# Kernel tuning notes

Hardware: AMD Instinct MI355X
Metric: run time of the kernel (lower is better)

The kernel has to match this reference:

```python
import jax, jax.numpy as jnp
import numpy as np

N = 50000     # nodes
E = 600000    # directed edges (avg degree 12)
F_IN = 128    # num_features
H = 128       # hidden_units
C = 16        # num_classes
G = 500       # graphs in batch


def setup_inputs() -> dict:
    key = jax.random.key(0)
    ks = jax.random.split(key, 6)
    x = jax.random.normal(ks[0], (N, F_IN), jnp.float32)
    edge_src = jax.random.randint(ks[1], (E,), 0, N, jnp.int32)
    edge_dst = jax.random.randint(ks[2], (E,), 0, N, jnp.int32)
    batch = jnp.sort(jax.random.randint(ks[3], (N,), 0, G, jnp.int32))
    W1 = jax.random.normal(ks[4], (F_IN, H), jnp.float32) / np.float32(np.sqrt(F_IN))
    b1 = jnp.zeros((H,), jnp.float32)
    W2 = jax.random.normal(ks[5], (H, C), jnp.float32) / np.float32(np.sqrt(H))
    b2 = jnp.zeros((C,), jnp.float32)
    return {"x": x, "W1": W1, "b1": b1, "W2": W2, "b2": b2,
            "edge_src": edge_src, "edge_dst": edge_dst, "batch": batch}


def _gcn_conv(x, W, b, src, dst, norm):
    # linear transform then normalized scatter-add aggregation (PyG GCNConv)
    h = x @ W                                   # [N, out]
    msg = h[src] * norm[:, None]                # [E+N, out]
    return jax.ops.segment_sum(msg, dst, num_segments=N) + b


def reference(x, W1, b1, W2, b2, edge_src, edge_dst, batch):
    # add self-loops
    loops = jnp.arange(N, dtype=edge_src.dtype)
    src = jnp.concatenate([edge_src, loops])
    dst = jnp.concatenate([edge_dst, loops])
    # symmetric normalization D^-1/2 A D^-1/2 (in-degree at targets)
    deg = jax.ops.segment_sum(jnp.ones_like(dst, jnp.float32), dst, num_segments=N)
    dis = jax.lax.rsqrt(deg)  # deg >= 1 because of self-loops
    norm = dis[src] * dis[dst]

    h = jax.nn.relu(_gcn_conv(x, W1, b1, src, dst, norm))
    h = _gcn_conv(h, W2, b2, src, dst, norm)

    # scatter_mean pooling over graphs
    counts = jax.ops.segment_sum(jnp.ones((N,), jnp.float32), batch, num_segments=G)
    pooled = jax.ops.segment_sum(h, batch, num_segments=G) / jnp.maximum(counts, 1.0)[:, None]
    return jax.nn.log_softmax(pooled, axis=1)
```

## Files before the change

### kernel.cpp

```cpp
#include <hip/hip_runtime.h>
#include <hip/hip_bf16.h>


#define NN 50000
#define EE 600000
#define FIN 128
#define HH 128
#define CC 16
#define GG 500
#define ETOT (EE + NN)
#define SBLK 196
#define WTS 140

typedef unsigned short ushort_t;
typedef unsigned int uint_t;

typedef __attribute__((ext_vector_type(8))) short bf16x8;
typedef __attribute__((ext_vector_type(8))) ushort_t u16x8;
typedef __attribute__((ext_vector_type(4))) ushort_t u16x4;
typedef __attribute__((ext_vector_type(4))) float f32x4;
typedef __attribute__((ext_vector_type(2))) float f32x2;

__device__ inline ushort_t f2bf(float f) {
    uint_t u = __float_as_uint(f);
    u = (u + 0x7FFFu + ((u >> 16) & 1u)) >> 16;
    return (ushort_t)u;
}
__device__ inline float bf2f(ushort_t b) {
    return __uint_as_float(((uint_t)b) << 16);
}
__device__ inline ushort_t f2h(float f) {
    _Float16 h = (_Float16)f; ushort_t u; __builtin_memcpy(&u, &h, 2); return u;
}
__device__ inline float h2f(ushort_t u) {
    _Float16 h; __builtin_memcpy(&h, &u, 2); return (float)h;
}

__global__ void init_kernel(int* cnt, float* pooled) {
    int i = blockIdx.x * blockDim.x + threadIdx.x;
    if (i < NN) cnt[i] = 0;
    if (i < GG * CC) pooled[i] = 0.0f;
}

__global__ void count_kernel(const int* __restrict__ edge_dst,
                             int* __restrict__ cnt, int* __restrict__ seq) {
    int idx = blockIdx.x * blockDim.x + threadIdx.x;
    if (idx < EE) seq[idx] = atomicAdd(&cnt[edge_dst[idx]], 1);
}

__global__ __launch_bounds__(256) void gemm1_kernel(const float* __restrict__ x,
                                                    const float* __restrict__ W1,
                                                    unsigned char* __restrict__ hb8) {
    __shared__ ushort_t xs[64 * 136];
    __shared__ ushort_t wt[128 * WTS];
    int t = threadIdx.x;
    int row0 = blockIdx.x * 64;
    for (int i = 0; i < 8; i++) {
        int slot = t + i * 256;
        int r = slot >> 5, k4 = slot & 31;
        int gr = row0 + r;
        float4 v = (gr < NN) ? ((const float4*)x)[gr * 32 + k4]
                             : make_float4(0.f, 0.f, 0.f, 0.f);
        u16x4 bv = { f2bf(v.x), f2bf(v.y), f2bf(v.z), f2bf(v.w) };
        *(u16x4*)(&xs[r * 136 + k4 * 4]) = bv;
    }
    for (int i = 0; i < 16; i++) {
        int idx = t + i * 256;
        int c = idx & 127, k4 = idx >> 7;
        u16x4 bv = { f2bf(W1[(4 * k4 + 0) * HH + c]),
                     f2bf(W1[(4 * k4 + 1) * HH + c]),
                     f2bf(W1[(4 * k4 + 2) * HH + c]),
                     f2bf(W1[(4 * k4 + 3) * HH + c]) };
        *(u16x4*)(&wt[c * WTS + k4 * 4]) = bv;
    }
    __syncthreads();

    int wave = t >> 6, lane = t & 63;
    int m = lane & 15, quad = lane >> 4;
    f32x4 acc[8];
    for (int ct = 0; ct < 8; ct++) acc[ct] = (f32x4)(0.0f);
    for (int ko = 0; ko < 4; ko++) {
        bf16x8 a = *(const bf16x8*)(&xs[(16 * wave + m) * 136 + ko * 32 + quad * 8]);
        for (int ct = 0; ct < 8; ct++) {
            bf16x8 b = *(const bf16x8*)(&wt[(ct * 16 + m) * WTS + ko * 32 + quad * 8]);
            acc[ct] = __builtin_amdgcn_mfma_f32_16x16x32_bf16(a, b, acc[ct], 0, 0, 0);
        }
    }
    for (int ct = 0; ct < 8; ct++) {
        int gcol = ct * 16 + m;
        for (int r = 0; r < 4; r++) {
            int grow = row0 + wave * 16 + quad * 4 + r;
            if (grow < NN) {
                int p = __builtin_amdgcn_cvt_pk_fp8_f32(acc[ct][r], 0.0f, 0, false);
                hb8[(size_t)grow * HH + gcol] = (unsigned char)(p & 0xFF);
            }
        }
    }
}

__device__ inline int block_excl_scan(int v, int t, int* total) {
    __shared__ int wsum[4];
    int lane = t & 63, wv = t >> 6;
    int inc = v;
    for (int off = 1; off < 64; off <<= 1) {
        int n = __shfl_up(inc, off);
        if (lane >= off) inc += n;
    }
    if (lane == 63) wsum[wv] = inc;
    __syncthreads();
    int off_w = 0;
    for (int w = 0; w < wv; w++) off_w += wsum[w];
    *total = wsum[0] + wsum[1] + wsum[2] + wsum[3];
    return off_w + inc - v;
}

__global__ __launch_bounds__(256) void scanA_kernel(const int* __restrict__ cnt,
                                                    int* __restrict__ rowptr,
                                                    float* __restrict__ dis,
                                                    int* __restrict__ bsum) {
    int t = threadIdx.x;
    int i = blockIdx.x * 256 + t;
    int d = 0;
    if (i < NN) {
        d = cnt[i] + 1;
        dis[i] = rsqrtf((float)d);
    }
    int total;
    int excl = block_excl_scan(d, t, &total);
    if (i < NN) rowptr[i] = excl;
    if (t == 0) bsum[blockIdx.x] = total;
}

__global__ __launch_bounds__(256) void scanBC_kernel(int* __restrict__ rowptr,
                                                     const int* __restrict__ bsum) {
    __shared__ int sb[256];
    int t = threadIdx.x;
    int v = (t < SBLK) ? bsum[t] : 0;
    int total;
    int ex = block_excl_scan(v, t, &total);
    sb[t] = ex;
    __syncthreads();
    int myoff = sb[blockIdx.x];
    int i = blockIdx.x * 256 + t;
    if (i < NN) rowptr[i] += myoff;
    if (blockIdx.x == 0 && t == 0) rowptr[NN] = ETOT;
}

__global__ void fill_kernel(const int* __restrict__ edge_src,
                            const int* __restrict__ edge_dst,
                            const float* __restrict__ dis,
                            const int* __restrict__ rowptr,
                            const int* __restrict__ seq,
                            uint_t* __restrict__ csr) {
    int idx = blockIdx.x * blockDim.x + threadIdx.x;
    if (idx < EE) {
        int s = edge_src[idx], d = edge_dst[idx];
        csr[rowptr[d] + seq[idx]] = (uint_t)s | ((uint_t)f2h(dis[s]) << 16);
    } else if (idx < ETOT) {
        int n = idx - EE;
        csr[rowptr[n + 1] - 1] = (uint_t)n | ((uint_t)f2h(dis[n]) << 16);
    }
}

__global__ __launch_bounds__(256) void agg1_kernel(const unsigned char* __restrict__ hb8,
                                                   const int* __restrict__ rowptr,
                                                   const uint_t* __restrict__ csr,
                                                   const float* __restrict__ dis,
                                                   const float* __restrict__ b1,
                                                   ushort_t* __restrict__ h1b) {
    int wave = threadIdx.x >> 6, lane = threadIdx.x & 63;
    int node = blockIdx.x * 4 + wave;
    int slot = lane >> 3, sub = lane & 7;
    int e0 = rowptr[node], e1 = rowptr[node + 1];
    float acc[16];
    for (int j = 0; j < 16; j++) acc[j] = 0.0f;
    for (int e = e0 + slot; e < e1; e += 16) {
        uint_t ent0 = csr[e];
        bool has2 = (e + 8) < e1;
        uint_t ent1 = has2 ? csr[e + 8] : ent0;
        uint4 hv0 = *(const uint4*)(hb8 + (size_t)(ent0 & 0xFFFFu) * HH + sub * 16);
        uint4 hv1 = has2 ? *(const uint4*)(hb8 + (size_t)(ent1 & 0xFFFFu) * HH + sub * 16)
                         : make_uint4(0, 0, 0, 0);
        float w0 = h2f((ushort_t)(ent0 >> 16));
        uint_t words0[4] = { hv0.x, hv0.y, hv0.z, hv0.w };
        for (int q = 0; q < 4; q++) {
            f32x2 lo = __builtin_amdgcn_cvt_pk_f32_fp8(words0[q], false);
            f32x2 hi = __builtin_amdgcn_cvt_pk_f32_fp8(words0[q], true);
            acc[q * 4 + 0] += w0 * lo[0];
            acc[q * 4 + 1] += w0 * lo[1];
            acc[q * 4 + 2] += w0 * hi[0];
            acc[q * 4 + 3] += w0 * hi[1];
        }
        if (has2) {
            float w1 = h2f((ushort_t)(ent1 >> 16));
            uint_t words1[4] = { hv1.x, hv1.y, hv1.z, hv1.w };
            for (int q = 0; q < 4; q++) {
                f32x2 lo = __builtin_amdgcn_cvt_pk_f32_fp8(words1[q], false);
                f32x2 hi = __builtin_amdgcn_cvt_pk_f32_fp8(words1[q], true);
                acc[q * 4 + 0] += w1 * lo[0];
                acc[q * 4 + 1] += w1 * lo[1];
                acc[q * 4 + 2] += w1 * hi[0];
                acc[q * 4 + 3] += w1 * hi[1];
            }
        }
    }
    for (int j = 0; j < 16; j++) {
        acc[j] += __shfl_xor(acc[j], 8);
        acc[j] += __shfl_xor(acc[j], 16);
        acc[j] += __shfl_xor(acc[j], 32);
    }
    if (slot == 0) {
        float dn = dis[node];
        const float4* b1v = (const float4*)(b1 + sub * 16);
        float4 bb[4] = { b1v[0], b1v[1], b1v[2], b1v[3] };
        const float* bbf = (const float*)bb;
        u16x8 o0, o1;
        for (int j = 0; j < 8; j++) {
            o0[j] = f2bf(fmaxf(dn * acc[j]     + bbf[j],     0.0f));
            o1[j] = f2bf(fmaxf(dn * acc[8 + j] + bbf[8 + j], 0.0f));
        }
        *(u16x8*)(h1b + (size_t)node * HH + sub * 16)     = o0;
        *(u16x8*)(h1b + (size_t)node * HH + sub * 16 + 8) = o1;
    }
}

__global__ __launch_bounds__(256) void gemm2_kernel(const ushort_t* __restrict__ h1b,
                                                    const float* __restrict__ W2,
                                                    ushort_t* __restrict__ h2b) {
    __shared__ ushort_t w2t[CC * 132];
    int t = threadIdx.x;
    for (int i = t; i < HH * CC; i += 256) {
        int k = i >> 4, m = i & 15;
        w2t[m * 132 + k] = f2bf(W2[i]);
    }
    __syncthreads();
    int wave = t >> 6, lane = t & 63;
    int m = lane & 15, quad = lane >> 4;
    int node0 = (blockIdx.x * 4 + wave) * 16;
    f32x4 acc = (f32x4)(0.0f);
    int arow = node0 + m;
    for (int ko = 0; ko < 4; ko++) {
        bf16x8 a = *(const bf16x8*)(h1b + (size_t)arow * HH + ko * 32 + quad * 8);
        bf16x8 b = *(const bf16x8*)(&w2t[m * 132 + ko * 32 + quad * 8]);
        acc = __builtin_amdgcn_mfma_f32_16x16x32_bf16(a, b, acc, 0, 0, 0);
    }
    for (int r = 0; r < 4; r++) {
        int grow = node0 + quad * 4 + r;
        h2b[(size_t)grow * CC + m] = f2bf(acc[r]);
    }
}

__global__ __launch_bounds__(1024) void agg2pool_kernel(const ushort_t* __restrict__ h2b,
                                                        const int* __restrict__ rowptr,
                                                        const uint_t* __restrict__ csr,
                                                        const float* __restrict__ dis,
                                                        const float* __restrict__ b2,
                                                        const int* __restrict__ batch,
                                                        float* __restrict__ pooled) {
    __shared__ float vals[16][16];
    __shared__ int gid[16];
    int wave = threadIdx.x >> 6, lane = threadIdx.x & 63;
    int node = blockIdx.x * 16 + wave;
    int slot = lane >> 3, sub = lane & 7;
    int e0 = rowptr[node], e1 = rowptr[node + 1];
    float a0 = 0.0f, a1 = 0.0f;
    for (int e = e0 + slot; e < e1; e += 16) {
        uint_t ent0 = csr[e];
        bool has2 = (e + 8) < e1;
        uint_t ent1 = has2 ? csr[e + 8] : ent0;
        uint_t p0 = *(const uint_t*)(h2b + (size_t)(ent0 & 0xFFFFu) * CC + sub * 2);
        uint_t p1 = has2 ? *(const uint_t*)(h2b + (size_t)(ent1 & 0xFFFFu) * CC + sub * 2) : 0;
        float w0 = h2f((ushort_t)(ent0 >> 16));
        a0 += w0 * bf2f((ushort_t)(p0 & 0xFFFFu));
        a1 += w0 * bf2f((ushort_t)(p0 >> 16));
        if (has2) {
            float w1 = h2f((ushort_t)(ent1 >> 16));
            a0 += w1 * bf2f((ushort_t)(p1 & 0xFFFFu));
            a1 += w1 * bf2f((ushort_t)(p1 >> 16));
        }
    }
    a0 += __shfl_xor(a0, 8); a0 += __shfl_xor(a0, 16); a0 += __shfl_xor(a0, 32);
    a1 += __shfl_xor(a1, 8); a1 += __shfl_xor(a1, 16); a1 += __shfl_xor(a1, 32);
    if (slot == 0) {
        float dn = dis[node];
        vals[wave][2 * sub]     = a0 * dn + b2[2 * sub];
        vals[wave][2 * sub + 1] = a1 * dn + b2[2 * sub + 1];
        if (sub == 0) gid[wave] = batch[node];
    }
    __syncthreads();
    if (threadIdx.x < 16) {
        int c = threadIdx.x;
        float run = 0.0f;
        for (int i = 0; i < 16; i++) {
            run += vals[i][c];
            if (i == 15 || gid[i + 1] != gid[i]) {
                atomicAdd(&pooled[gid[i] * CC + c], run);
                run = 0.0f;
            }
        }
    }
}

__global__ void lsm_kernel(const float* __restrict__ pooled,
                           const int* __restrict__ batch,
                           float* __restrict__ out) {
    int idx = blockIdx.x * blockDim.x + threadIdx.x;
    int g = idx >> 4, c = idx & 15;
    if (g >= GG) return;
    int lo = 0, hi = NN;
    while (lo < hi) { int mid = (lo + hi) >> 1; if (batch[mid] < g) lo = mid + 1; else hi = mid; }
    int lo2 = lo, hi2 = NN;
    while (lo2 < hi2) { int mid = (lo2 + hi2) >> 1; if (batch[mid] < g + 1) lo2 = mid + 1; else hi2 = mid; }
    float cnt = (float)(lo2 - lo);
    float v = pooled[g * CC + c] / fmaxf(cnt, 1.0f);
    float m = v;
    for (int off = 8; off >= 1; off >>= 1) m = fmaxf(m, __shfl_xor(m, off, 16));
    float s = expf(v - m);
    for (int off = 8; off >= 1; off >>= 1) s += __shfl_xor(s, off, 16);
    out[g * CC + c] = v - m - logf(s);
}

extern "C" void kernel_launch(void* const* d_in, const int* in_sizes, int n_in,
                              void* d_out, int out_size, void* d_ws, size_t ws_size,
                              hipStream_t stream) {
    const float* x  = (const float*)d_in[0];
    const float* W1 = (const float*)d_in[1];
    const float* b1 = (const float*)d_in[2];
    const float* W2 = (const float*)d_in[3];
    const float* b2 = (const float*)d_in[4];
    const int* edge_src = (const int*)d_in[5];
    const int* edge_dst = (const int*)d_in[6];
    const int* batch    = (const int*)d_in[7];
    float* out = (float*)d_out;

    char* ws = (char*)d_ws;
    size_t off = 0;
    auto alloc = [&](size_t bytes) {
        void* p = ws + off;
        off += (bytes + 255) & ~size_t(255);
        return p;
    };
    int*   cnt     = (int*)  alloc(NN * 4);
    float* dis     = (float*)alloc(NN * 4);
    int*   rowptr  = (int*)  alloc((NN + 1) * 4);
    int*   seq     = (int*)  alloc(EE * 4);
    int*   bsum    = (int*)  alloc(SBLK * 4);
    uint_t* csr    = (uint_t*)alloc((size_t)ETOT * 4);
    unsigned char* hb8 = (unsigned char*)alloc((size_t)NN * HH);
    ushort_t* h1b  = (ushort_t*)alloc((size_t)NN * HH * 2);
    ushort_t* h2b  = (ushort_t*)alloc((size_t)NN * CC * 2);
    float* pooled  = (float*)alloc(GG * CC * 4);

    const int B = 256;
    init_kernel<<<(NN + B - 1) / B, B, 0, stream>>>(cnt, pooled);
    count_kernel<<<(EE + B - 1) / B, B, 0, stream>>>(edge_dst, cnt, seq);
    gemm1_kernel<<<(NN + 63) / 64, B, 0, stream>>>(x, W1, hb8);
    scanA_kernel<<<SBLK, B, 0, stream>>>(cnt, rowptr, dis, bsum);
    scanBC_kernel<<<SBLK, B, 0, stream>>>(rowptr, bsum);
    fill_kernel<<<(ETOT + B - 1) / B, B, 0, stream>>>(edge_src, edge_dst, dis,
                                                      rowptr, seq, csr);
    agg1_kernel<<<NN / 4, B, 0, stream>>>(hb8, rowptr, csr, dis, b1, h1b);
    gemm2_kernel<<<(NN + 63) / 64, B, 0, stream>>>(h1b, W2, h2b);
    agg2pool_kernel<<<NN / 16, 1024, 0, stream>>>(h2b, rowptr, csr, dis, b2, batch, pooled);
    lsm_kernel<<<(GG * CC + B - 1) / B, B, 0, stream>>>(pooled, batch, out);
}
```

Before: 199.9 us.

## Fuse layer-1 aggregation with layer-2 GEMM and precompute graph counts

Merges agg1 and gemm2 into one kernel. Each 4-node block writes its bf16 hidden rows to shared memory and wave 0 runs the 16x16 MFMA against W2 staged in LDS. This removes the 12.8 MB h1b round trip through global memory and one kernel launch. In exchange, every block now converts W2 and runs an MFMA that is only a quarter full (4 of 16 rows), which adds per-block work and a barrier. Graph counts are now accumulated with atomics in count_kernel instead of binary searches in lsm_kernel, and a few loads in agg2pool are hoisted ahead of the edge loop.

```diff
diff --git a/kernel.cpp b/kernel.cpp
--- a/kernel.cpp
+++ b/kernel.cpp
@@ -36,16 +36,20 @@
     _Float16 h; __builtin_memcpy(&h, &u, 2); return (float)h;
 }
 
-__global__ void init_kernel(int* cnt, float* pooled) {
+__global__ void init_kernel(int* cnt, float* pooled, int* gcnt) {
     int i = blockIdx.x * blockDim.x + threadIdx.x;
     if (i < NN) cnt[i] = 0;
     if (i < GG * CC) pooled[i] = 0.0f;
+    if (i < GG) gcnt[i] = 0;
 }
 
 __global__ void count_kernel(const int* __restrict__ edge_dst,
-                             int* __restrict__ cnt, int* __restrict__ seq) {
+                             const int* __restrict__ batch,
+                             int* __restrict__ cnt, int* __restrict__ seq,
+                             int* __restrict__ gcnt) {
     int idx = blockIdx.x * blockDim.x + threadIdx.x;
     if (idx < EE) seq[idx] = atomicAdd(&cnt[edge_dst[idx]], 1);
+    if (idx < NN) atomicAdd(&gcnt[batch[idx]], 1);
 }
 
 __global__ __launch_bounds__(256) void gemm1_kernel(const float* __restrict__ x,
@@ -162,16 +166,21 @@
     }
 }
 
-__global__ __launch_bounds__(256) void agg1_kernel(const unsigned char* __restrict__ hb8,
-                                                   const int* __restrict__ rowptr,
-                                                   const uint_t* __restrict__ csr,
-                                                   const float* __restrict__ dis,
-                                                   const float* __restrict__ b1,
-                                                   ushort_t* __restrict__ h1b) {
-    int wave = threadIdx.x >> 6, lane = threadIdx.x & 63;
+__global__ __launch_bounds__(256) void agg1g2_kernel(const unsigned char* __restrict__ hb8,
+                                                     const int* __restrict__ rowptr,
+                                                     const uint_t* __restrict__ csr,
+                                                     const float* __restrict__ dis,
+                                                     const float* __restrict__ b1,
+                                                     const float* __restrict__ W2,
+                                                     ushort_t* __restrict__ h2b) {
+    __shared__ ushort_t h1s[16 * 136];
+    __shared__ ushort_t w2t[CC * 132];
+    int t = threadIdx.x;
+    int wave = t >> 6, lane = t & 63;
     int node = blockIdx.x * 4 + wave;
     int slot = lane >> 3, sub = lane & 7;
     int e0 = rowptr[node], e1 = rowptr[node + 1];
+    float dn = dis[node];
     float acc[16];
     for (int j = 0; j < 16; j++) acc[j] = 0.0f;
     for (int e = e0 + slot; e < e1; e += 16) {
@@ -204,13 +213,16 @@
             }
         }
     }
+    for (int i = t; i < HH * CC; i += 256) {
+        int k = i >> 4, m = i & 15;
+        w2t[m * 132 + k] = f2bf(W2[i]);
+    }
     for (int j = 0; j < 16; j++) {
         acc[j] += __shfl_xor(acc[j], 8);
         acc[j] += __shfl_xor(acc[j], 16);
         acc[j] += __shfl_xor(acc[j], 32);
     }
     if (slot == 0) {
-        float dn = dis[node];
         const float4* b1v = (const float4*)(b1 + sub * 16);
         float4 bb[4] = { b1v[0], b1v[1], b1v[2], b1v[3] };
         const float* bbf = (const float*)bb;
@@ -219,34 +231,24 @@
             o0[j] = f2bf(fmaxf(dn * acc[j]     + bbf[j],     0.0f));
             o1[j] = f2bf(fmaxf(dn * acc[8 + j] + bbf[8 + j], 0.0f));
         }
-        *(u16x8*)(h1b + (size_t)node * HH + sub * 16)     = o0;
-        *(u16x8*)(h1b + (size_t)node * HH + sub * 16 + 8) = o1;
-    }
-}
-
-__global__ __launch_bounds__(256) void gemm2_kernel(const ushort_t* __restrict__ h1b,
-                                                    const float* __restrict__ W2,
-                                                    ushort_t* __restrict__ h2b) {
-    __shared__ ushort_t w2t[CC * 132];
-    int t = threadIdx.x;
-    for (int i = t; i < HH * CC; i += 256) {
-        int k = i >> 4, m = i & 15;
-        w2t[m * 132 + k] = f2bf(W2[i]);
-    }
-    __syncthreads();
-    int wave = t >> 6, lane = t & 63;
-    int m = lane & 15, quad = lane >> 4;
-    int node0 = (blockIdx.x * 4 + wave) * 16;
-    f32x4 acc = (f32x4)(0.0f);
-    int arow = node0 + m;
-    for (int ko = 0; ko < 4; ko++) {
-        bf16x8 a = *(const bf16x8*)(h1b + (size_t)arow * HH + ko * 32 + quad * 8);
-        bf16x8 b = *(const bf16x8*)(&w2t[m * 132 + ko * 32 + quad * 8]);
-        acc = __builtin_amdgcn_mfma_f32_16x16x32_bf16(a, b, acc, 0, 0, 0);
-    }
-    for (int r = 0; r < 4; r++) {
-        int grow = node0 + quad * 4 + r;
-        h2b[(size_t)grow * CC + m] = f2bf(acc[r]);
+        *(u16x8*)(&h1s[wave * 136 + sub * 16])     = o0;
+        *(u16x8*)(&h1s[wave * 136 + sub * 16 + 8]) = o1;
+    }
+    __syncthreads();
+    if (wave == 0) {
+        int m = lane & 15, quad = lane >> 4;
+        f32x4 acc2 = (f32x4)(0.0f);
+        for (int ko = 0; ko < 4; ko++) {
+            bf16x8 a = *(const bf16x8*)(&h1s[m * 136 + ko * 32 + quad * 8]);
+            bf16x8 b = *(const bf16x8*)(&w2t[m * 132 + ko * 32 + quad * 8]);
+            acc2 = __builtin_amdgcn_mfma_f32_16x16x32_bf16(a, b, acc2, 0, 0, 0);
+        }
+        if (quad == 0) {
+            int node0 = blockIdx.x * 4;
+            for (int r = 0; r < 4; r++) {
+                h2b[(size_t)(node0 + r) * CC + m] = f2bf(acc2[r]);
+            }
+        }
     }
 }
 
@@ -263,6 +265,9 @@
     int node = blockIdx.x * 16 + wave;
     int slot = lane >> 3, sub = lane & 7;
     int e0 = rowptr[node], e1 = rowptr[node + 1];
+    float dn = dis[node];
+    int   bg = batch[node];
+    float b20 = b2[2 * sub], b21 = b2[2 * sub + 1];
     float a0 = 0.0f, a1 = 0.0f;
     for (int e = e0 + slot; e < e1; e += 16) {
         uint_t ent0 = csr[e];
@@ -282,10 +287,9 @@
     a0 += __shfl_xor(a0, 8); a0 += __shfl_xor(a0, 16); a0 += __shfl_xor(a0, 32);
     a1 += __shfl_xor(a1, 8); a1 += __shfl_xor(a1, 16); a1 += __shfl_xor(a1, 32);
     if (slot == 0) {
-        float dn = dis[node];
-        vals[wave][2 * sub]     = a0 * dn + b2[2 * sub];
-        vals[wave][2 * sub + 1] = a1 * dn + b2[2 * sub + 1];
-        if (sub == 0) gid[wave] = batch[node];
+        vals[wave][2 * sub]     = a0 * dn + b20;
+        vals[wave][2 * sub + 1] = a1 * dn + b21;
+        if (sub == 0) gid[wave] = bg;
     }
     __syncthreads();
     if (threadIdx.x < 16) {
@@ -302,16 +306,12 @@
 }
 
 __global__ void lsm_kernel(const float* __restrict__ pooled,
-                           const int* __restrict__ batch,
+                           const int* __restrict__ gcnt,
                            float* __restrict__ out) {
     int idx = blockIdx.x * blockDim.x + threadIdx.x;
     int g = idx >> 4, c = idx & 15;
     if (g >= GG) return;
-    int lo = 0, hi = NN;
-    while (lo < hi) { int mid = (lo + hi) >> 1; if (batch[mid] < g) lo = mid + 1; else hi = mid; }
-    int lo2 = lo, hi2 = NN;
-    while (lo2 < hi2) { int mid = (lo2 + hi2) >> 1; if (batch[mid] < g + 1) lo2 = mid + 1; else hi2 = mid; }
-    float cnt = (float)(lo2 - lo);
+    float cnt = (float)gcnt[g];
     float v = pooled[g * CC + c] / fmaxf(cnt, 1.0f);
     float m = v;
     for (int off = 8; off >= 1; off >>= 1) m = fmaxf(m, __shfl_xor(m, off, 16));
@@ -347,20 +347,19 @@
     int*   bsum    = (int*)  alloc(SBLK * 4);
     uint_t* csr    = (uint_t*)alloc((size_t)ETOT * 4);
     unsigned char* hb8 = (unsigned char*)alloc((size_t)NN * HH);
-    ushort_t* h1b  = (ushort_t*)alloc((size_t)NN * HH * 2);
     ushort_t* h2b  = (ushort_t*)alloc((size_t)NN * CC * 2);
     float* pooled  = (float*)alloc(GG * CC * 4);
+    int*   gcnt    = (int*)  alloc(GG * 4);
 
     const int B = 256;
-    init_kernel<<<(NN + B - 1) / B, B, 0, stream>>>(cnt, pooled);
-    count_kernel<<<(EE + B - 1) / B, B, 0, stream>>>(edge_dst, cnt, seq);
+    init_kernel<<<(NN + B - 1) / B, B, 0, stream>>>(cnt, pooled, gcnt);
+    count_kernel<<<(EE + B - 1) / B, B, 0, stream>>>(edge_dst, batch, cnt, seq, gcnt);
     gemm1_kernel<<<(NN + 63) / 64, B, 0, stream>>>(x, W1, hb8);
     scanA_kernel<<<SBLK, B, 0, stream>>>(cnt, rowptr, dis, bsum);
     scanBC_kernel<<<SBLK, B, 0, stream>>>(rowptr, bsum);
     fill_kernel<<<(ETOT + B - 1) / B, B, 0, stream>>>(edge_src, edge_dst, dis,
                                                       rowptr, seq, csr);
-    agg1_kernel<<<NN / 4, B, 0, stream>>>(hb8, rowptr, csr, dis, b1, h1b);
-    gemm2_kernel<<<(NN + 63) / 64, B, 0, stream>>>(h1b, W2, h2b);
+    agg1g2_kernel<<<NN / 4, B, 0, stream>>>(hb8, rowptr, csr, dis, b1, W2, h2b);
     agg2pool_kernel<<<NN / 16, 1024, 0, stream>>>(h2b, rowptr, csr, dis, b2, batch, pooled);
-    lsm_kernel<<<(GG * CC + B - 1) / B, B, 0, stream>>>(pooled, batch, out);
-}
+    lsm_kernel<<<(GG * CC + B - 1) / B, B, 0, stream>>>(pooled, gcnt, out);
+}
```

Result: slower. 224.1 us (+12.1%).

## Fuse edge counting into GEMM1 launch and precompute graph boundaries in scan

Applied to the files above, without the earlier changes.

Merges the degree-count atomics and the first GEMM into one heterogeneous launch, so the block ranges run concurrently and one kernel launch is removed. Graph start offsets are computed in the scan kernel, replacing two binary searches per thread in the log-softmax kernel. Loads of dis, batch and bias are hoisted before the aggregation loops, and gemm2 stores gain a bounds guard, with the buffers padded to match. The fused kernel now gives every block, including the counting blocks, the GEMM's large shared-memory allocation, which may reduce occupancy for the atomic part.

```diff
diff --git a/kernel.cpp b/kernel.cpp
--- a/kernel.cpp
+++ b/kernel.cpp
@@ -11,6 +11,7 @@
 #define ETOT (EE + NN)
 #define SBLK 196
 #define WTS 140
+#define CBLK ((EE + 255) / 256)
 
 typedef unsigned short ushort_t;
 typedef unsigned int uint_t;
@@ -42,19 +43,21 @@
     if (i < GG * CC) pooled[i] = 0.0f;
 }
 
-__global__ void count_kernel(const int* __restrict__ edge_dst,
-                             int* __restrict__ cnt, int* __restrict__ seq) {
-    int idx = blockIdx.x * blockDim.x + threadIdx.x;
-    if (idx < EE) seq[idx] = atomicAdd(&cnt[edge_dst[idx]], 1);
-}
-
-__global__ __launch_bounds__(256) void gemm1_kernel(const float* __restrict__ x,
-                                                    const float* __restrict__ W1,
-                                                    unsigned char* __restrict__ hb8) {
+__global__ __launch_bounds__(256) void cg1_kernel(const int* __restrict__ edge_dst,
+                                                  int* __restrict__ cnt,
+                                                  int* __restrict__ seq,
+                                                  const float* __restrict__ x,
+                                                  const float* __restrict__ W1,
+                                                  unsigned char* __restrict__ hb8) {
     __shared__ ushort_t xs[64 * 136];
     __shared__ ushort_t wt[128 * WTS];
+    if (blockIdx.x < CBLK) {
+        int idx = blockIdx.x * 256 + threadIdx.x;
+        if (idx < EE) seq[idx] = atomicAdd(&cnt[edge_dst[idx]], 1);
+        return;
+    }
     int t = threadIdx.x;
-    int row0 = blockIdx.x * 64;
+    int row0 = (blockIdx.x - CBLK) * 64;
     for (int i = 0; i < 8; i++) {
         int slot = t + i * 256;
         int r = slot >> 5, k4 = slot & 31;
@@ -117,13 +120,21 @@
 __global__ __launch_bounds__(256) void scanA_kernel(const int* __restrict__ cnt,
                                                     int* __restrict__ rowptr,
                                                     float* __restrict__ dis,
-                                                    int* __restrict__ bsum) {
+                                                    int* __restrict__ bsum,
+                                                    const int* __restrict__ batch,
+                                                    int* __restrict__ gstart) {
     int t = threadIdx.x;
     int i = blockIdx.x * 256 + t;
     int d = 0;
     if (i < NN) {
         d = cnt[i] + 1;
         dis[i] = rsqrtf((float)d);
+        int b = batch[i];
+        int bp = (i == 0) ? -1 : batch[i - 1];
+        for (int g = bp + 1; g <= b; ++g) gstart[g] = i;
+        if (i == NN - 1) {
+            for (int g = b + 1; g <= GG; ++g) gstart[g] = NN;
+        }
     }
     int total;
     int excl = block_excl_scan(d, t, &total);
@@ -172,6 +183,7 @@
     int node = blockIdx.x * 4 + wave;
     int slot = lane >> 3, sub = lane & 7;
     int e0 = rowptr[node], e1 = rowptr[node + 1];
+    float dn = dis[node];
     float acc[16];
     for (int j = 0; j < 16; j++) acc[j] = 0.0f;
     for (int e = e0 + slot; e < e1; e += 16) {
@@ -210,7 +222,6 @@
         acc[j] += __shfl_xor(acc[j], 32);
     }
     if (slot == 0) {
-        float dn = dis[node];
         const float4* b1v = (const float4*)(b1 + sub * 16);
         float4 bb[4] = { b1v[0], b1v[1], b1v[2], b1v[3] };
         const float* bbf = (const float*)bb;
@@ -246,7 +257,7 @@
     }
     for (int r = 0; r < 4; r++) {
         int grow = node0 + quad * 4 + r;
-        h2b[(size_t)grow * CC + m] = f2bf(acc[r]);
+        if (grow < NN) h2b[(size_t)grow * CC + m] = f2bf(acc[r]);
     }
 }
 
@@ -263,6 +274,9 @@
     int node = blockIdx.x * 16 + wave;
     int slot = lane >> 3, sub = lane & 7;
     int e0 = rowptr[node], e1 = rowptr[node + 1];
+    float dn = dis[node];
+    int   bg = batch[node];
+    float b20 = b2[2 * sub], b21 = b2[2 * sub + 1];
     float a0 = 0.0f, a1 = 0.0f;
     for (int e = e0 + slot; e < e1; e += 16) {
         uint_t ent0 = csr[e];
@@ -282,10 +296,9 @@
     a0 += __shfl_xor(a0, 8); a0 += __shfl_xor(a0, 16); a0 += __shfl_xor(a0, 32);
     a1 += __shfl_xor(a1, 8); a1 += __shfl_xor(a1, 16); a1 += __shfl_xor(a1, 32);
     if (slot == 0) {
-        float dn = dis[node];
-        vals[wave][2 * sub]     = a0 * dn + b2[2 * sub];
-        vals[wave][2 * sub + 1] = a1 * dn + b2[2 * sub + 1];
-        if (sub == 0) gid[wave] = batch[node];
+        vals[wave][2 * sub]     = a0 * dn + b20;
+        vals[wave][2 * sub + 1] = a1 * dn + b21;
+        if (sub == 0) gid[wave] = bg;
     }
     __syncthreads();
     if (threadIdx.x < 16) {
@@ -302,16 +315,12 @@
 }
 
 __global__ void lsm_kernel(const float* __restrict__ pooled,
-                           const int* __restrict__ batch,
+                           const int* __restrict__ gstart,
                            float* __restrict__ out) {
     int idx = blockIdx.x * blockDim.x + threadIdx.x;
     int g = idx >> 4, c = idx & 15;
     if (g >= GG) return;
-    int lo = 0, hi = NN;
-    while (lo < hi) { int mid = (lo + hi) >> 1; if (batch[mid] < g) lo = mid + 1; else hi = mid; }
-    int lo2 = lo, hi2 = NN;
-    while (lo2 < hi2) { int mid = (lo2 + hi2) >> 1; if (batch[mid] < g + 1) lo2 = mid + 1; else hi2 = mid; }
-    float cnt = (float)(lo2 - lo);
+    float cnt = (float)(gstart[g + 1] - gstart[g]);
     float v = pooled[g * CC + c] / fmaxf(cnt, 1.0f);
     float m = v;
     for (int off = 8; off >= 1; off >>= 1) m = fmaxf(m, __shfl_xor(m, off, 16));
@@ -347,20 +356,20 @@
     int*   bsum    = (int*)  alloc(SBLK * 4);
     uint_t* csr    = (uint_t*)alloc((size_t)ETOT * 4);
     unsigned char* hb8 = (unsigned char*)alloc((size_t)NN * HH);
-    ushort_t* h1b  = (ushort_t*)alloc((size_t)NN * HH * 2);
-    ushort_t* h2b  = (ushort_t*)alloc((size_t)NN * CC * 2);
+    ushort_t* h1b  = (ushort_t*)alloc(((size_t)NN + 64) * HH * 2);
+    ushort_t* h2b  = (ushort_t*)alloc(((size_t)NN + 64) * CC * 2);
     float* pooled  = (float*)alloc(GG * CC * 4);
+    int*   gstart  = (int*)  alloc((GG + 1) * 4);
 
     const int B = 256;
     init_kernel<<<(NN + B - 1) / B, B, 0, stream>>>(cnt, pooled);
-    count_kernel<<<(EE + B - 1) / B, B, 0, stream>>>(edge_dst, cnt, seq);
-    gemm1_kernel<<<(NN + 63) / 64, B, 0, stream>>>(x, W1, hb8);
-    scanA_kernel<<<SBLK, B, 0, stream>>>(cnt, rowptr, dis, bsum);
+    cg1_kernel<<<CBLK + (NN + 63) / 64, B, 0, stream>>>(edge_dst, cnt, seq, x, W1, hb8);
+    scanA_kernel<<<SBLK, B, 0, stream>>>(cnt, rowptr, dis, bsum, batch, gstart);
     scanBC_kernel<<<SBLK, B, 0, stream>>>(rowptr, bsum);
     fill_kernel<<<(ETOT + B - 1) / B, B, 0, stream>>>(edge_src, edge_dst, dis,
                                                       rowptr, seq, csr);
     agg1_kernel<<<NN / 4, B, 0, stream>>>(hb8, rowptr, csr, dis, b1, h1b);
     gemm2_kernel<<<(NN + 63) / 64, B, 0, stream>>>(h1b, W2, h2b);
     agg2pool_kernel<<<NN / 16, 1024, 0, stream>>>(h2b, rowptr, csr, dis, b2, batch, pooled);
-    lsm_kernel<<<(GG * CC + B - 1) / B, B, 0, stream>>>(pooled, batch, out);
-}
+    lsm_kernel<<<(GG * CC + B - 1) / B, B, 0, stream>>>(pooled, gstart, out);
+}
```

Measured after the change: 190.1 us. -4.9%, faster.
